# Performance work log

Hardware: AMD Instinct MI355X
Metric: run time of the kernel (lower is better)

Reference implementation:

```python
import jax, jax.numpy as jnp
import numpy as np

B, L, T = 2, 512, 1024
E, H = 2560, 128
HW = E // H  # head_width = 20

def setup_inputs() -> dict:
    key = jax.random.key(0)
    k1, k2, k3, k4, k5 = jax.random.split(key, 5)
    x = jax.random.normal(k1, (B, L, T), dtype=jnp.float32)
    mask = jax.random.randint(k2, (B, L), 0, 2) > 0  # bool, 1=valid
    bias = jax.random.normal(k3, (B, L, L, H), dtype=jnp.float32)
    W_up = jax.random.normal(k4, (E, T), dtype=jnp.float32) * 0.02
    W_proj = jax.random.normal(k5, (2 * E, E), dtype=jnp.float32) * 0.02
    return {"x": x, "mask": mask, "bias": bias, "W_up": W_up, "W_proj": W_proj}

def reference(x, mask, bias, W_up, W_proj):
    # dimensionup: [B,L,T] -> [B,L,E]
    xe = jnp.einsum('blt,et->ble', x, W_up)
    # proj: [B,L,E] -> [B,L,2E], rearrange '(h c)' -> [B,H,L,2*HW]
    t = jnp.einsum('ble,fe->blf', xe, W_proj)
    t = t.reshape(B, L, H, 2 * HW).transpose(0, 2, 1, 3)  # [B,H,L,2*HW]
    q, k = t[..., :HW], t[..., HW:]
    q = q * (HW ** -0.5)
    a = jnp.einsum('bhqc,bhkc->bhqk', q, k)           # [B,H,Lq,Lk]
    a = a + jnp.transpose(bias, (0, 3, 1, 2))          # bias: [B,Lq,Lk,H] -> [B,H,Lq,Lk]
    a = jnp.where(mask[:, None, None, :], a, 0.0)      # mask keys; 0 where padding
    return jnp.transpose(a, (0, 2, 3, 1))              # [B,Lq,Lk,H]
```

## Files before the change

kernel.cpp:

```cpp
#include <hip/hip_runtime.h>
#include <hip/hip_bf16.h>
#include <hip/hip_fp16.h>

static constexpr int Bc = 2, Lc = 512, Tc = 1024, Ec = 2560, Hc = 128, HWc = 20;
static constexpr int F2 = 2 * Ec;
static constexpr float QSCALE = 0.22360679774997896f;

typedef _Float16 half8 __attribute__((ext_vector_type(8)));
typedef _Float16 half4v __attribute__((ext_vector_type(4)));
typedef float floatx4 __attribute__((ext_vector_type(4)));

__device__ __forceinline__ void gl_lds16(const _Float16* g, _Float16* l) {
  __builtin_amdgcn_global_load_lds(
      (const __attribute__((address_space(1))) void*)g,
      (__attribute__((address_space(3))) void*)l, 16, 0, 0);
}

__global__ void decode_mask_k(const unsigned* __restrict__ mraw, int* __restrict__ mdec) {
  __shared__ int flag;
  if (threadIdx.x == 0) flag = 0;
  __syncthreads();
  if (threadIdx.x < 256) {
    unsigned v = mraw[threadIdx.x];
    if (v > 1u) atomicOr(&flag, 1);
  }
  __syncthreads();
  int t = threadIdx.x;
  int v;
  if (flag) v = (int)((const unsigned char*)mraw)[t];
  else      v = ((const int*)mraw)[t];
  mdec[t] = (v != 0) ? 1 : 0;
}

__global__ void cvt_f32_f16_k(const float* __restrict__ in, _Float16* __restrict__ out, int n8) {
  int i = blockIdx.x * blockDim.x + threadIdx.x;
  int gs = gridDim.x * blockDim.x;
  for (; i < n8; i += gs) {
    const floatx4* p = (const floatx4*)(in + (size_t)i * 8);
    floatx4 a = p[0], b = p[1];
    half8 hv;
#pragma unroll
    for (int c = 0; c < 4; ++c) { hv[c] = (_Float16)a[c]; hv[4 + c] = (_Float16)b[c]; }
    *(half8*)(out + (size_t)i * 8) = hv;
  }
}

__global__ void cvt_wproj_k(const float* __restrict__ in, _Float16* __restrict__ out, int n8) {
  int i = blockIdx.x * blockDim.x + threadIdx.x;
  int gs = gridDim.x * blockDim.x;
  for (; i < n8; i += gs) {
    int row = (int)(((long)i * 8) / Ec);
    float sc = ((row % 40) < HWc) ? QSCALE : 1.0f;
    const floatx4* p = (const floatx4*)(in + (size_t)i * 8);
    floatx4 a = p[0], b = p[1];
    half8 hv;
#pragma unroll
    for (int c = 0; c < 4; ++c) { hv[c] = (_Float16)(a[c] * sc); hv[4 + c] = (_Float16)(b[c] * sc); }
    *(half8*)(out + (size_t)i * 8) = hv;
  }
}

__global__ __launch_bounds__(256) void gemm_nt_f16(
    const _Float16* __restrict__ A, const _Float16* __restrict__ B,
    _Float16* __restrict__ C, int M, int N, int K) {
  __shared__ __align__(16) _Float16 As[4096];
  __shared__ __align__(16) _Float16 Bs[4096];
  const int tid = threadIdx.x;
  const int w = tid >> 6;
  const int l = tid & 63;
  const int wr = w >> 1, wc = w & 1;
  const long m0 = (long)blockIdx.y * 128;
  const long n0 = (long)blockIdx.x * 128;

  floatx4 acc[4][4];
#pragma unroll
  for (int i = 0; i < 4; ++i)
#pragma unroll
    for (int j = 0; j < 4; ++j) acc[i][j] = (floatx4)0.0f;

  const int rA0 = w * 16 + (l >> 2);
  const int rA1 = rA0 + 64;
  const int c16 = l & 3;
  const _Float16* gA0 = A + (m0 + rA0) * (long)K + ((c16 ^ ((rA0 >> 1) & 3)) * 8);
  const _Float16* gA1 = A + (m0 + rA1) * (long)K + ((c16 ^ ((rA1 >> 1) & 3)) * 8);
  const _Float16* gB0 = B + (n0 + rA0) * (long)K + ((c16 ^ ((rA0 >> 1) & 3)) * 8);
  const _Float16* gB1 = B + (n0 + rA1) * (long)K + ((c16 ^ ((rA1 >> 1) & 3)) * 8);
  _Float16* lA0 = As + w * 512;
  _Float16* lA1 = As + 2048 + w * 512;
  _Float16* lB0 = Bs + w * 512;
  _Float16* lB1 = Bs + 2048 + w * 512;

  int aoff[4], boff[4];
  const int g = l >> 4;
#pragma unroll
  for (int mi = 0; mi < 4; ++mi) {
    int row = wr * 64 + mi * 16 + (l & 15);
    aoff[mi] = row * 32 + ((g ^ ((row >> 1) & 3)) * 8);
    int rowb = wc * 64 + mi * 16 + (l & 15);
    boff[mi] = rowb * 32 + ((g ^ ((rowb >> 1) & 3)) * 8);
  }

  for (int k0 = 0; k0 < K; k0 += 32) {
    gl_lds16(gA0 + k0, lA0);
    gl_lds16(gA1 + k0, lA1);
    gl_lds16(gB0 + k0, lB0);
    gl_lds16(gB1 + k0, lB1);
    __syncthreads();
    half8 a[4], b[4];
#pragma unroll
    for (int mi = 0; mi < 4; ++mi) a[mi] = *(const half8*)(As + aoff[mi]);
#pragma unroll
    for (int ni = 0; ni < 4; ++ni) b[ni] = *(const half8*)(Bs + boff[ni]);
#pragma unroll
    for (int mi = 0; mi < 4; ++mi)
#pragma unroll
      for (int ni = 0; ni < 4; ++ni)
        acc[mi][ni] = __builtin_amdgcn_mfma_f32_16x16x32_f16(a[mi], b[ni], acc[mi][ni], 0, 0, 0);
    __syncthreads();
  }

#pragma unroll
  for (int mi = 0; mi < 4; ++mi)
#pragma unroll
    for (int ni = 0; ni < 4; ++ni)
#pragma unroll
      for (int r = 0; r < 4; ++r) {
        long row = m0 + wr * 64 + mi * 16 + ((l >> 4) * 4 + r);
        long col = n0 + wc * 64 + ni * 16 + (l & 15);
        C[row * (long)N + col] = (_Float16)acc[mi][ni][r];
      }
}

__global__ __launch_bounds__(256) void scores_kernel(
    const _Float16* __restrict__ T, const float* __restrict__ bias,
    const int* __restrict__ mdec, float* __restrict__ out) {
  const int tid = threadIdx.x;
  const int h = tid & 127;
  const int jo = tid >> 7;
  const int bx = blockIdx.x;
  const int b = bx >> 10;
  const int rem = bx & 1023;
  const int i0 = (rem >> 3) * 4;
  const int j0 = (rem & 7) * 64;

  float q[4][20];
#pragma unroll
  for (int ii = 0; ii < 4; ++ii) {
    const _Float16* qp = T + (size_t)((b * Lc + i0 + ii) * F2 + h * 40);
    half8 v0 = *(const half8*)qp;
    half8 v1 = *(const half8*)(qp + 8);
    half4v v2 = *(const half4v*)(qp + 16);
#pragma unroll
    for (int c = 0; c < 8; ++c) { q[ii][c] = (float)v0[c]; q[ii][8 + c] = (float)v1[c]; }
#pragma unroll
    for (int c = 0; c < 4; ++c) q[ii][16 + c] = (float)v2[c];
  }

  for (int it = 0; it < 32; ++it) {
    const int j = j0 + it * 2 + jo;
    const int mv = mdec[b * Lc + j];
    const size_t ob = (((size_t)(b * Lc + i0) * Lc + j) << 7) + h;
    if (mv) {
      const _Float16* kp = T + (size_t)((b * Lc + j) * F2 + h * 40 + 20);
      half4v k0 = *(const half4v*)kp;
      half4v k1 = *(const half4v*)(kp + 4);
      half4v k2 = *(const half4v*)(kp + 8);
      half4v k3 = *(const half4v*)(kp + 12);
      half4v k4 = *(const half4v*)(kp + 16);
      float kv[20];
#pragma unroll
      for (int c = 0; c < 4; ++c) {
        kv[c] = (float)k0[c]; kv[4 + c] = (float)k1[c]; kv[8 + c] = (float)k2[c];
        kv[12 + c] = (float)k3[c]; kv[16 + c] = (float)k4[c];
      }
#pragma unroll
      for (int ii = 0; ii < 4; ++ii) {
        float s = 0.f;
#pragma unroll
        for (int c = 0; c < 20; ++c) s = fmaf(q[ii][c], kv[c], s);
        const size_t o = ob + (size_t)ii * (Lc * Hc);
        out[o] = s + bias[o];
      }
    } else {
#pragma unroll
      for (int ii = 0; ii < 4; ++ii) out[ob + (size_t)ii * (Lc * Hc)] = 0.0f;
    }
  }
}

extern "C" void kernel_launch(void* const* d_in, const int* in_sizes, int n_in,
                              void* d_out, int out_size, void* d_ws, size_t ws_size,
                              hipStream_t stream) {
  const float* x      = (const float*)d_in[0];
  const void*  mask   = d_in[1];
  const float* bias   = (const float*)d_in[2];
  const float* W_up   = (const float*)d_in[3];
  const float* W_proj = (const float*)d_in[4];
  float* out = (float*)d_out;

  char* ws = (char*)d_ws;
  int*      mdec    = (int*)ws;
  _Float16* x_h     = (_Float16*)(ws + 4096);
  _Float16* wup_h   = (_Float16*)(ws + 4096 + 2097152);
  _Float16* wproj_h = (_Float16*)(ws + 4096 + 2097152 + 5242880);
  _Float16* xe_h    = (_Float16*)(ws + 4096 + 2097152 + 5242880 + 26214400);
  _Float16* t_h     = (_Float16*)(ws + 4096 + 2097152 + 5242880 + 26214400 + 5242880);

  decode_mask_k<<<1, 1024, 0, stream>>>((const unsigned*)mask, mdec);
  cvt_f32_f16_k<<<512, 256, 0, stream>>>(x, x_h, 131072);
  cvt_f32_f16_k<<<1280, 256, 0, stream>>>(W_up, wup_h, 327680);
  cvt_wproj_k<<<2048, 256, 0, stream>>>(W_proj, wproj_h, 1638400);

  gemm_nt_f16<<<dim3(2560 / 128, 1024 / 128), 256, 0, stream>>>(x_h, wup_h, xe_h, 1024, 2560, 1024);
  gemm_nt_f16<<<dim3(5120 / 128, 1024 / 128), 256, 0, stream>>>(xe_h, wproj_h, t_h, 1024, 5120, 2560);

  scores_kernel<<<2048, 256, 0, stream>>>(t_h, bias, mdec, out);
}
```

Baseline: 615.1 us.

## Double-buffer GEMM LDS tiles, use 8 waves per block, fuse conversion kernels

The three fp32-to-fp16 conversion kernels are merged into one launch. The GEMM is rewritten to use 512 threads (8 waves, each computing a 64x32 subtile) with a double-buffered LDS ring. The next k-tile is prefetched while the current one feeds the MFMAs, cutting one barrier per iteration. A 1D grid with an XCD-aware block swizzle groups neighbouring output tiles on the same die for cache locality. The cost is twice the LDS per block and more waves per tile, which may lower the number of blocks per CU.

Measured after the change: 605.4 us. No clear change (-1.6%).

```diff
diff --git a/kernel.cpp b/kernel.cpp
--- a/kernel.cpp
+++ b/kernel.cpp
@@ -32,102 +32,108 @@
   mdec[t] = (v != 0) ? 1 : 0;
 }
 
-__global__ void cvt_f32_f16_k(const float* __restrict__ in, _Float16* __restrict__ out, int n8) {
+__global__ void cvt_all_k(const float* __restrict__ x, const float* __restrict__ wup,
+                          const float* __restrict__ wproj, _Float16* __restrict__ xh,
+                          _Float16* __restrict__ wuph, _Float16* __restrict__ wprojh) {
+  const int NX = 131072, NU = 327680, NP = 1638400;
   int i = blockIdx.x * blockDim.x + threadIdx.x;
   int gs = gridDim.x * blockDim.x;
-  for (; i < n8; i += gs) {
-    const floatx4* p = (const floatx4*)(in + (size_t)i * 8);
+  for (; i < NX + NU + NP; i += gs) {
+    const float* src; _Float16* dst; int idx; float sc = 1.0f;
+    if (i < NX) { src = x; dst = xh; idx = i; }
+    else if (i < NX + NU) { src = wup; dst = wuph; idx = i - NX; }
+    else {
+      src = wproj; dst = wprojh; idx = i - NX - NU;
+      int row = (int)(((long)idx * 8) / Ec);
+      if ((row % 40) < HWc) sc = QSCALE;
+    }
+    const floatx4* p = (const floatx4*)(src + (size_t)idx * 8);
     floatx4 a = p[0], b = p[1];
     half8 hv;
 #pragma unroll
-    for (int c = 0; c < 4; ++c) { hv[c] = (_Float16)a[c]; hv[4 + c] = (_Float16)b[c]; }
-    *(half8*)(out + (size_t)i * 8) = hv;
-  }
-}
-
-__global__ void cvt_wproj_k(const float* __restrict__ in, _Float16* __restrict__ out, int n8) {
-  int i = blockIdx.x * blockDim.x + threadIdx.x;
-  int gs = gridDim.x * blockDim.x;
-  for (; i < n8; i += gs) {
-    int row = (int)(((long)i * 8) / Ec);
-    float sc = ((row % 40) < HWc) ? QSCALE : 1.0f;
-    const floatx4* p = (const floatx4*)(in + (size_t)i * 8);
-    floatx4 a = p[0], b = p[1];
-    half8 hv;
-#pragma unroll
     for (int c = 0; c < 4; ++c) { hv[c] = (_Float16)(a[c] * sc); hv[4 + c] = (_Float16)(b[c] * sc); }
-    *(half8*)(out + (size_t)i * 8) = hv;
-  }
-}
-
-__global__ __launch_bounds__(256) void gemm_nt_f16(
+    *(half8*)(dst + (size_t)idx * 8) = hv;
+  }
+}
+
+__global__ __launch_bounds__(512) void gemm_nt_f16_v2(
     const _Float16* __restrict__ A, const _Float16* __restrict__ B,
-    _Float16* __restrict__ C, int M, int N, int K) {
-  __shared__ __align__(16) _Float16 As[4096];
-  __shared__ __align__(16) _Float16 Bs[4096];
+    _Float16* __restrict__ C, int M, int N, int K, int nbx) {
+  __shared__ __align__(16) _Float16 As[2][4096];
+  __shared__ __align__(16) _Float16 Bs[2][4096];
   const int tid = threadIdx.x;
   const int w = tid >> 6;
   const int l = tid & 63;
-  const int wr = w >> 1, wc = w & 1;
-  const long m0 = (long)blockIdx.y * 128;
-  const long n0 = (long)blockIdx.x * 128;
-
-  floatx4 acc[4][4];
+  const int wr = w >> 2, wc = w & 3;
+
+  const int nwg = gridDim.x;
+  const int cpx = nwg >> 3;
+  const int id = blockIdx.x;
+  const int swz = (id & 7) * cpx + (id >> 3);
+  const long m0 = (long)(swz / nbx) * 128;
+  const long n0 = (long)(swz % nbx) * 128;
+
+  floatx4 acc[4][2];
 #pragma unroll
   for (int i = 0; i < 4; ++i)
 #pragma unroll
-    for (int j = 0; j < 4; ++j) acc[i][j] = (floatx4)0.0f;
-
-  const int rA0 = w * 16 + (l >> 2);
-  const int rA1 = rA0 + 64;
-  const int c16 = l & 3;
-  const _Float16* gA0 = A + (m0 + rA0) * (long)K + ((c16 ^ ((rA0 >> 1) & 3)) * 8);
-  const _Float16* gA1 = A + (m0 + rA1) * (long)K + ((c16 ^ ((rA1 >> 1) & 3)) * 8);
-  const _Float16* gB0 = B + (n0 + rA0) * (long)K + ((c16 ^ ((rA0 >> 1) & 3)) * 8);
-  const _Float16* gB1 = B + (n0 + rA1) * (long)K + ((c16 ^ ((rA1 >> 1) & 3)) * 8);
-  _Float16* lA0 = As + w * 512;
-  _Float16* lA1 = As + 2048 + w * 512;
-  _Float16* lB0 = Bs + w * 512;
-  _Float16* lB1 = Bs + 2048 + w * 512;
-
-  int aoff[4], boff[4];
+    for (int j = 0; j < 2; ++j) acc[i][j] = (floatx4)0.0f;
+
+  const int r = tid >> 2;
+  const int c16l = (tid & 3) ^ ((r >> 1) & 3);
+  const _Float16* gA = A + (m0 + r) * (long)K + c16l * 8;
+  const _Float16* gB = B + (n0 + r) * (long)K + c16l * 8;
+  _Float16* lA = (_Float16*)As + w * 512;
+  _Float16* lB = (_Float16*)Bs + w * 512;
+
+  int aoff[4], boff[2];
   const int g = l >> 4;
 #pragma unroll
   for (int mi = 0; mi < 4; ++mi) {
     int row = wr * 64 + mi * 16 + (l & 15);
     aoff[mi] = row * 32 + ((g ^ ((row >> 1) & 3)) * 8);
-    int rowb = wc * 64 + mi * 16 + (l & 15);
-    boff[mi] = rowb * 32 + ((g ^ ((rowb >> 1) & 3)) * 8);
-  }
-
-  for (int k0 = 0; k0 < K; k0 += 32) {
-    gl_lds16(gA0 + k0, lA0);
-    gl_lds16(gA1 + k0, lA1);
-    gl_lds16(gB0 + k0, lB0);
-    gl_lds16(gB1 + k0, lB1);
-    __syncthreads();
-    half8 a[4], b[4];
-#pragma unroll
-    for (int mi = 0; mi < 4; ++mi) a[mi] = *(const half8*)(As + aoff[mi]);
-#pragma unroll
-    for (int ni = 0; ni < 4; ++ni) b[ni] = *(const half8*)(Bs + boff[ni]);
+  }
+#pragma unroll
+  for (int ni = 0; ni < 2; ++ni) {
+    int col = wc * 32 + ni * 16 + (l & 15);
+    boff[ni] = col * 32 + ((g ^ ((col >> 1) & 3)) * 8);
+  }
+
+  const int nt = K >> 5;
+  gl_lds16(gA, lA);
+  gl_lds16(gB, lB);
+  __syncthreads();
+  int cur = 0;
+  for (int t = 0; t < nt; ++t) {
+    if (t + 1 < nt) {
+      gl_lds16(gA + (t + 1) * 32, lA + ((cur ^ 1) << 12));
+      gl_lds16(gB + (t + 1) * 32, lB + ((cur ^ 1) << 12));
+    }
+    const _Float16* Ab = (const _Float16*)As + (cur << 12);
+    const _Float16* Bb = (const _Float16*)Bs + (cur << 12);
+    half8 a[4], b[2];
+#pragma unroll
+    for (int mi = 0; mi < 4; ++mi) a[mi] = *(const half8*)(Ab + aoff[mi]);
+#pragma unroll
+    for (int ni = 0; ni < 2; ++ni) b[ni] = *(const half8*)(Bb + boff[ni]);
 #pragma unroll
     for (int mi = 0; mi < 4; ++mi)
 #pragma unroll
-      for (int ni = 0; ni < 4; ++ni)
+      for (int ni = 0; ni < 2; ++ni)
         acc[mi][ni] = __builtin_amdgcn_mfma_f32_16x16x32_f16(a[mi], b[ni], acc[mi][ni], 0, 0, 0);
     __syncthreads();
+    cur ^= 1;
   }
 
 #pragma unroll
   for (int mi = 0; mi < 4; ++mi)
 #pragma unroll
-    for (int ni = 0; ni < 4; ++ni)
-#pragma unroll
-      for (int r = 0; r < 4; ++r) {
-        long row = m0 + wr * 64 + mi * 16 + ((l >> 4) * 4 + r);
-        long col = n0 + wc * 64 + ni * 16 + (l & 15);
-        C[row * (long)N + col] = (_Float16)acc[mi][ni][r];
+    for (int ni = 0; ni < 2; ++ni)
+#pragma unroll
+      for (int rr = 0; rr < 4; ++rr) {
+        long row = m0 + wr * 64 + mi * 16 + ((l >> 4) * 4 + rr);
+        long col = n0 + wc * 32 + ni * 16 + (l & 15);
+        C[row * (long)N + col] = (_Float16)acc[mi][ni][rr];
       }
 }
 
@@ -207,12 +213,10 @@
   _Float16* t_h     = (_Float16*)(ws + 4096 + 2097152 + 5242880 + 26214400 + 5242880);
 
   decode_mask_k<<<1, 1024, 0, stream>>>((const unsigned*)mask, mdec);
-  cvt_f32_f16_k<<<512, 256, 0, stream>>>(x, x_h, 131072);
-  cvt_f32_f16_k<<<1280, 256, 0, stream>>>(W_up, wup_h, 327680);
-  cvt_wproj_k<<<2048, 256, 0, stream>>>(W_proj, wproj_h, 1638400);
-
-  gemm_nt_f16<<<dim3(2560 / 128, 1024 / 128), 256, 0, stream>>>(x_h, wup_h, xe_h, 1024, 2560, 1024);
-  gemm_nt_f16<<<dim3(5120 / 128, 1024 / 128), 256, 0, stream>>>(xe_h, wproj_h, t_h, 1024, 5120, 2560);
+  cvt_all_k<<<2048, 256, 0, stream>>>(x, W_up, W_proj, x_h, wup_h, wproj_h);
+
+  gemm_nt_f16_v2<<<160, 512, 0, stream>>>(x_h, wup_h, xe_h, 1024, 2560, 1024, 20);
+  gemm_nt_f16_v2<<<320, 512, 0, stream>>>(xe_h, wproj_h, t_h, 1024, 5120, 2560, 40);
 
   scores_kernel<<<2048, 256, 0, stream>>>(t_h, bias, mdec, out);
 }
```
